# Kernel tuning notes

Hardware: AMD Instinct MI355X
Metric: run time of the kernel (lower is better)

Reference implementation:

```python
import jax, jax.numpy as jnp
import numpy as np

L = 2000          # number of residues (sequence length)
FEATURES_L = 2048 # config.features_L pad target
W = 7             # config.window_size
D = 54            # per-residue feature dim after bert_lin
H = 3             # attention heads
HD = D // H       # head dim = 18
CH = 32           # conv hidden channels
KS = (3, 5, 7)    # config.kernels


def setup_inputs() -> dict:
    key = jax.random.key(0)
    ks = jax.random.split(key, 20)
    n = lambda k, s, sc=0.02: jax.random.normal(k, s, jnp.float32) * sc
    return {
        'beft_f': jax.random.normal(ks[0], (L, 1024), jnp.float32),
        'pssm_f': jax.random.normal(ks[1], (L, 20), jnp.float32),
        'hmm_f': jax.random.normal(ks[2], (L, 30), jnp.float32),
        'dssp_f': jax.random.normal(ks[3], (L, 14), jnp.float32),
        'W_bert': n(ks[4], (1024, D)), 'b_bert': jnp.zeros((D,), jnp.float32),
        'ln_g1': jnp.ones((D,), jnp.float32), 'ln_b1': jnp.zeros((D,), jnp.float32),
        'ln_g2': jnp.ones((D,), jnp.float32), 'ln_b2': jnp.zeros((D,), jnp.float32),
        'conv1_w': n(ks[5], (CH, 1, 3, 1), 0.1), 'conv1_b': n(ks[6], (CH,), 0.1),
        'prelu_a': jnp.array(0.25, jnp.float32),
        'conv2_w': n(ks[7], (CH, 1, 5, 1), 0.1), 'conv2_b': n(ks[8], (CH,), 0.1),
        'conv3_w': n(ks[9], (CH, 1, 7, 1), 0.1), 'conv3_b': n(ks[10], (CH,), 0.1),
        'W1': n(ks[11], (972, 256)), 'b1': jnp.zeros((256,), jnp.float32),
        'W2': n(ks[12], (CH * 256, 256)), 'b2': jnp.zeros((256,), jnp.float32),
    }


def _ln(x, g, b, eps=1e-5):
    m = x.mean(-1, keepdims=True)
    v = ((x - m) ** 2).mean(-1, keepdims=True)
    return (x - m) * jax.lax.rsqrt(v + eps) * g + b


def _attn(x, g, b):
    # x: (L, W, D); no qkv projections, no 1/sqrt(d) scaling (as in source)
    qh = x.reshape(x.shape[0], W, H, HD)
    s = jnp.einsum('bqhd,bkhd->bhqk', qh, qh)
    p = jax.nn.softmax(s, axis=-1)
    o = jnp.einsum('bhqk,bkhd->bqhd', p, qh).reshape(x.shape[0], W, D)
    return _ln(o, g, b)


def _conv_branch(x, w, bias, k, act):
    pad = (k - 1) // 2
    c = jax.lax.conv_general_dilated(x, w, (1, 1), ((pad, pad), (0, 0)),
                                     dimension_numbers=('NCHW', 'OIHW', 'NCHW'))
    c = act(c + bias[None, :, None, None])
    c = jax.lax.reduce_window(c, -jnp.inf, jax.lax.max,
                              (1, 1, k, 1), (1, 1, 1, 1), 'VALID')
    return c.reshape(c.shape[0], CH, -1)  # (FEATURES_L, 32, (W-k+1)*2D)


def _forward(beft_f, W_bert, b_bert, ln_g1, ln_b1, ln_g2, ln_b2,
             conv1_w, conv1_b, prelu_a, conv2_w, conv2_b, conv3_w, conv3_b,
             W1, b1, W2, b2):
    f = beft_f @ W_bert + b_bert  # (L, 54)
    # sliding-window gather replicating the source python loop exactly:
    # interior rows i in (W, L-W): window = f[i-4 : i+3]; boundary rows: [f[i], 0...0]
    i = jnp.arange(L)
    j = jnp.arange(W)
    gidx = jnp.clip(i[:, None] - (W // 2 + 1) + j[None, :], 0, L - 1)
    win_int = f[gidx]                                   # (L, 7, 54)
    win_bnd = jnp.zeros((L, W, D), f.dtype).at[:, 0].set(f)
    boundary = (i <= W) | (i + W >= L)
    new_f = jnp.where(boundary[:, None, None], win_bnd, win_int)
    sf = _attn(new_f, ln_g1, ln_b1)
    sf = _attn(sf, ln_g2, ln_b2)
    cat = jnp.concatenate([new_f, sf], axis=2)          # (L, 7, 108)
    x = jnp.pad(cat, ((0, FEATURES_L - L), (0, 0), (0, 0)))[:, None]  # (FL,1,7,108)
    prelu = lambda z: jnp.where(z >= 0, z, prelu_a * z)
    feats = jnp.concatenate([
        _conv_branch(x, conv1_w, conv1_b, KS[0], prelu),
        _conv_branch(x, conv2_w, conv2_b, KS[1], jax.nn.relu),
        _conv_branch(x, conv3_w, conv3_b, KS[2], jax.nn.relu)], axis=2)  # (FL,32,972)
    y = feats[:L] @ W1 + b1                             # (L, 32, 256)
    y = y.reshape(L, CH * 256) @ W2 + b2                # (L, 256)
    return jnp.where(y >= 0, y, 0.01 * y)               # leaky_relu


def reference(beft_f, pssm_f, hmm_f, dssp_f, W_bert, b_bert, ln_g1, ln_b1,
              ln_g2, ln_b2, conv1_w, conv1_b, prelu_a, conv2_w, conv2_b,
              conv3_w, conv3_b, W1, b1, W2, b2):
    # pssm_f / hmm_f / dssp_f are accepted but unused in the source forward
    return _forward(beft_f, W_bert, b_bert, ln_g1, ln_b1, ln_g2, ln_b2,
                    conv1_w, conv1_b, prelu_a, conv2_w, conv2_b,
                    conv3_w, conv3_b, W1, b1, W2, b2)
```

## Files before the change

### kernel.cpp

```cpp
#include <hip/hip_runtime.h>

#define L_RES 2000
#define DF 54
#define WIN 7

typedef short bf16x8 __attribute__((ext_vector_type(8)));
typedef float f32x4 __attribute__((ext_vector_type(4)));
typedef unsigned short ushort8v __attribute__((ext_vector_type(8)));

__device__ __forceinline__ unsigned short f2bf(float f) {
    unsigned int u = __float_as_uint(f);
    unsigned int r = (u + 0x7FFFu + ((u >> 16) & 1u)) >> 16;
    return (unsigned short)r;
}
__device__ __forceinline__ float bf2f(unsigned short h) {
    return __uint_as_float(((unsigned int)h) << 16);
}
__device__ __forceinline__ void gload16(const unsigned short* g, unsigned short* l) {
    __builtin_amdgcn_global_load_lds(
        (const __attribute__((address_space(1))) void*)g,
        (__attribute__((address_space(3))) void*)l, 16, 0, 0);
}

__global__ __launch_bounds__(256) void b2t_build(const float* __restrict__ Wb,
                                                 unsigned short* __restrict__ B2T) {
    int idx = blockIdx.x * 256 + threadIdx.x;
    int n = idx / 3072, col = idx % 3072;
    int seg = col >> 10, k = col & 1023;
    unsigned short r = 0;
    if (n < DF) {
        float v = Wb[(size_t)k * DF + n];
        unsigned short hi = f2bf(v);
        r = (seg < 2) ? hi : f2bf(v - bf2f(hi));
    }
    B2T[idx] = r;
}

__global__ __launch_bounds__(256) void bert_mfma(const float* __restrict__ beft,
                                                 const unsigned short* __restrict__ B2T,
                                                 float* __restrict__ bpart) {
    __shared__ unsigned short ldsA[128 * 64];
    __shared__ unsigned short ldsB[64 * 64];
    int t = threadIdx.x, w = t >> 6, lane = t & 63;
    int m0 = blockIdx.x * 128;
    int z = blockIdx.y;
    int koff = z * 768;
    int wr = w >> 1, wc = w & 1;
    int arow = lane & 15, kgrp = lane >> 4;

    int cj[4], aD[4];
    const float* aF[4];
    bool vald[4];
    #pragma unroll
    for (int j = 0; j < 4; ++j) {
        int s = j * 256 + t, r = s >> 3, c = s & 7;
        cj[j] = c;
        aD[j] = r * 64 + ((c ^ (r & 7)) * 8);
        vald[j] = (m0 + r) < L_RES;
        aF[j] = beft + (size_t)(vald[j] ? (m0 + r) : 0) * 1024;
    }
    const unsigned short* bS[2]; int bD[2];
    #pragma unroll
    for (int j = 0; j < 2; ++j) {
        int s = j * 256 + t, r = s >> 3, c = s & 7;
        bS[j] = B2T + koff + (size_t)r * 3072 + c * 8;
        bD[j] = r * 64 + ((c ^ (r & 7)) * 8);
    }
    f32x4 acc[4][2];
    #pragma unroll
    for (int mi = 0; mi < 4; ++mi)
        #pragma unroll
        for (int ni = 0; ni < 2; ++ni) acc[mi][ni] = (f32x4)(0.f);

    f32x4 va0[4], va1[4];
    ushort8v vb[2];
    #pragma unroll
    for (int j = 0; j < 4; ++j) {
        int x = koff + cj[j] * 8;
        int bc = x & 1023;
        va0[j] = *(const f32x4*)(aF[j] + bc);
        va1[j] = *(const f32x4*)(aF[j] + bc + 4);
    }
    #pragma unroll
    for (int j = 0; j < 2; ++j) vb[j] = *(const ushort8v*)(bS[j]);

    for (int ks = 0; ks < 12; ++ks) {
        __syncthreads();
        #pragma unroll
        for (int j = 0; j < 4; ++j) {
            int x = koff + ks * 64 + cj[j] * 8;
            int seg = x >> 10;
            ushort8v v;
            #pragma unroll
            for (int e = 0; e < 8; ++e) {
                float val = (e < 4) ? va0[j][e] : va1[j][e - 4];
                if (!vald[j]) val = 0.f;
                unsigned short hi = f2bf(val);
                v[e] = (seg == 1) ? f2bf(val - bf2f(hi)) : hi;
            }
            *(ushort8v*)&ldsA[aD[j]] = v;
        }
        #pragma unroll
        for (int j = 0; j < 2; ++j) *(ushort8v*)&ldsB[bD[j]] = vb[j];
        __syncthreads();
        if (ks + 1 < 12) {
            #pragma unroll
            for (int j = 0; j < 4; ++j) {
                int x = koff + (ks + 1) * 64 + cj[j] * 8;
                int bc = x & 1023;
                va0[j] = *(const f32x4*)(aF[j] + bc);
                va1[j] = *(const f32x4*)(aF[j] + bc + 4);
            }
            #pragma unroll
            for (int j = 0; j < 2; ++j) vb[j] = *(const ushort8v*)(bS[j] + (ks + 1) * 64);
        }
        #pragma unroll
        for (int kk = 0; kk < 2; ++kk) {
            int chunk = kk * 4 + kgrp;
            bf16x8 af[4], bfr[2];
            #pragma unroll
            for (int mi = 0; mi < 4; ++mi) {
                int rl = wr * 64 + mi * 16 + arow;
                af[mi] = *(const bf16x8*)&ldsA[rl * 64 + ((chunk ^ (rl & 7)) * 8)];
            }
            #pragma unroll
            for (int ni = 0; ni < 2; ++ni) {
                int rl = wc * 32 + ni * 16 + arow;
                bfr[ni] = *(const bf16x8*)&ldsB[rl * 64 + ((chunk ^ (rl & 7)) * 8)];
            }
            #pragma unroll
            for (int mi = 0; mi < 4; ++mi)
                #pragma unroll
                for (int ni = 0; ni < 2; ++ni)
                    acc[mi][ni] = __builtin_amdgcn_mfma_f32_16x16x32_bf16(af[mi], bfr[ni], acc[mi][ni], 0, 0, 0);
        }
    }
    #pragma unroll
    for (int ni = 0; ni < 2; ++ni) {
        int n = wc * 32 + ni * 16 + arow;
        #pragma unroll
        for (int mi = 0; mi < 4; ++mi)
            #pragma unroll
            for (int r = 0; r < 4; ++r) {
                int m = m0 + wr * 64 + mi * 16 + kgrp * 4 + r;
                bpart[((size_t)z * 2048 + m) * 64 + n] = acc[mi][ni][r];
            }
    }
}

__global__ __launch_bounds__(64) void bert_reduce(const float* __restrict__ bpart,
                                                  const float* __restrict__ bb,
                                                  float* __restrict__ f) {
    int l = blockIdx.x, n = threadIdx.x;
    if (n < DF) {
        float s = bb[n];
        #pragma unroll
        for (int z = 0; z < 4; ++z) s += bpart[((size_t)z * 2048 + l) * 64 + n];
        f[(size_t)l * DF + n] = s;
    }
}

__device__ __forceinline__ void attn_layer(const float (*in)[DF], float (*out)[DF],
                                           float (*s)[WIN][WIN],
                                           const float* __restrict__ g,
                                           const float* __restrict__ b,
                                           float* mm, float* vv, int t) {
    for (int idx = t; idx < 3 * WIN * WIN; idx += 64) {
        int h = idx / 49, r = idx % 49, q = r / WIN, k = r % WIN;
        float sum = 0.f;
        #pragma unroll
        for (int d = 0; d < 18; ++d) sum = fmaf(in[q][h * 18 + d], in[k][h * 18 + d], sum);
        s[h][q][k] = sum;
    }
    __syncthreads();
    for (int idx = t; idx < 3 * WIN; idx += 64) {
        int h = idx / WIN, q = idx % WIN;
        float mx = s[h][q][0];
        #pragma unroll
        for (int k = 1; k < WIN; ++k) mx = fmaxf(mx, s[h][q][k]);
        float e[WIN], sum = 0.f;
        #pragma unroll
        for (int k = 0; k < WIN; ++k) { e[k] = expf(s[h][q][k] - mx); sum += e[k]; }
        float inv = 1.f / sum;
        #pragma unroll
        for (int k = 0; k < WIN; ++k) s[h][q][k] = e[k] * inv;
    }
    __syncthreads();
    for (int idx = t; idx < WIN * DF; idx += 64) {
        int q = idx / DF, c = idx % DF, h = c / 18;
        float sum = 0.f;
        #pragma unroll
        for (int k = 0; k < WIN; ++k) sum = fmaf(s[h][q][k], in[k][c], sum);
        out[q][c] = sum;
    }
    __syncthreads();
    for (int q = t; q < WIN; q += 64) {
        float m = 0.f;
        for (int c = 0; c < DF; ++c) m += out[q][c];
        m *= (1.f / DF);
        float v = 0.f;
        for (int c = 0; c < DF; ++c) { float d0 = out[q][c] - m; v = fmaf(d0, d0, v); }
        v *= (1.f / DF);
        mm[q] = m; vv[q] = rsqrtf(v + 1e-5f);
    }
    __syncthreads();
    for (int idx = t; idx < WIN * DF; idx += 64) {
        int q = idx / DF, c = idx % DF;
        out[q][c] = (out[q][c] - mm[q]) * vv[q] * g[c] + b[c];
    }
    __syncthreads();
}

__global__ __launch_bounds__(64) void window_attn(const float* __restrict__ f,
                                                  const float* __restrict__ g1,
                                                  const float* __restrict__ b1,
                                                  const float* __restrict__ g2,
                                                  const float* __restrict__ b2,
                                                  float* __restrict__ cat) {
    int l = blockIdx.x;
    int t = threadIdx.x;
    __shared__ float w[WIN][DF], o1[WIN][DF], o2[WIN][DF];
    __shared__ float s[3][WIN][WIN];
    __shared__ float mm[WIN], vv[WIN];
    bool boundary = (l <= WIN) || (l + WIN >= L_RES);
    for (int idx = t; idx < WIN * DF; idx += 64) {
        int j = idx / DF, d = idx % DF;
        w[j][d] = boundary ? (j == 0 ? f[(size_t)l * DF + d] : 0.f)
                           : f[(size_t)(l - 4 + j) * DF + d];
    }
    __syncthreads();
    attn_layer(w, o1, s, g1, b1, mm, vv, t);
    attn_layer(o1, o2, s, g2, b2, mm, vv, t);
    for (int idx = t; idx < WIN * DF; idx += 64) {
        int j = idx / DF, d = idx % DF;
        cat[(size_t)l * 756 + j * 108 + d] = w[j][d];
        cat[(size_t)l * 756 + j * 108 + DF + d] = o2[j][d];
    }
}

__global__ __launch_bounds__(256) void transpose_to_bf16(const float* __restrict__ src,
                                                         unsigned short* __restrict__ dst,
                                                         int M, int N, int Mpad) {
    __shared__ float tile[32][33];
    int m0 = blockIdx.x * 32, n0 = blockIdx.y * 32;
    int c = threadIdx.x % 32, r0 = threadIdx.x / 32;
    #pragma unroll
    for (int rr = 0; rr < 4; ++rr) {
        int r = r0 + rr * 8, m = m0 + r;
        tile[r][c] = (m < M) ? src[(size_t)m * N + n0 + c] : 0.f;
    }
    __syncthreads();
    #pragma unroll
    for (int rr = 0; rr < 4; ++rr) {
        int r = r0 + rr * 8;
        dst[(size_t)(n0 + r) * Mpad + m0 + c] = f2bf(tile[c][r]);
    }
}

__global__ __launch_bounds__(256) void w1tp_build(const float* __restrict__ W1,
                                                  unsigned short* __restrict__ P) {
    int idx = blockIdx.x * 256 + threadIdx.x;
    int e = idx & 7, l = (idx >> 3) & 63, g = (idx >> 9) & 31, nb = idx >> 14;
    int ks = g >> 1, kk = g & 1;
    int n = nb * 16 + (l & 15);
    int k = ks * 64 + kk * 32 + (l >> 4) * 8 + e;
    P[idx] = (k < 972) ? f2bf(W1[(size_t)k * 256 + n]) : (unsigned short)0;
}

__global__ __launch_bounds__(256) void conv_pool(
        const float* __restrict__ cat,
        const float* __restrict__ c1w, const float* __restrict__ c1b,
        const float* __restrict__ pa_p,
        const float* __restrict__ c2w, const float* __restrict__ c2b,
        const float* __restrict__ c3w, const float* __restrict__ c3b,
        unsigned short* __restrict__ Ap, int lbase) {
    int bid = blockIdx.x;
    int b = bid >> 2;
    int ch0 = (bid & 3) * 8;
    int l0 = lbase + b * 4;
    int t = threadIdx.x;
    __shared__ float catl[4 * 756];
    for (int i = t; i < 3024; i += 256) catl[i] = cat[(size_t)l0 * 756 + i];
    __syncthreads();
    float pa = pa_p[0];
    unsigned short* base = Ap + (size_t)b * 128 * 1024;
    int res = t >> 6, dp = t & 63;
    if (dp < 54) {
        int d0 = dp * 2;
        const float* cr = catl + res * 756;
        float colA[WIN], colB[WIN];
        #pragma unroll
        for (int h = 0; h < WIN; ++h) {
            colA[h] = cr[h * 108 + d0];
            colB[h] = cr[h * 108 + d0 + 1];
        }
        for (int c = ch0; c < ch0 + 8; ++c) {
            unsigned short* Arow = base + (size_t)(res * 32 + c) * 1024;
            {
                float w0 = c1w[c * 3], w1 = c1w[c * 3 + 1], w2 = c1w[c * 3 + 2];
                float bb = c1b[c];
                float vA[WIN], vB[WIN];
                #pragma unroll
                for (int h = 0; h < WIN; ++h) {
                    float sA = bb, sB = bb;
                    if (h >= 1) { sA = fmaf(w0, colA[h - 1], sA); sB = fmaf(w0, colB[h - 1], sB); }
                    sA = fmaf(w1, colA[h], sA); sB = fmaf(w1, colB[h], sB);
                    if (h <= 5) { sA = fmaf(w2, colA[h + 1], sA); sB = fmaf(w2, colB[h + 1], sB); }
                    vA[h] = sA >= 0.f ? sA : pa * sA;
                    vB[h] = sB >= 0.f ? sB : pa * sB;
                }
                #pragma unroll
                for (int p = 0; p < 5; ++p) {
                    unsigned int ua = f2bf(fmaxf(fmaxf(vA[p], vA[p + 1]), vA[p + 2]));
                    unsigned int ub = f2bf(fmaxf(fmaxf(vB[p], vB[p + 1]), vB[p + 2]));
                    *(unsigned int*)&Arow[p * 108 + d0] = ua | (ub << 16);
                }
            }
            {
                float wg[5], bb = c2b[c];
                #pragma unroll
                for (int x = 0; x < 5; ++x) wg[x] = c2w[c * 5 + x];
                float vA[WIN], vB[WIN];
                #pragma unroll
                for (int h = 0; h < WIN; ++h) {
                    float sA = bb, sB = bb;
                    #pragma unroll
                    for (int x = 0; x < 5; ++x) {
                        int hh = h + x - 2;
                        if (hh >= 0 && hh <= 6) {
                            sA = fmaf(wg[x], colA[hh], sA);
                            sB = fmaf(wg[x], colB[hh], sB);
                        }
                    }
                    vA[h] = fmaxf(sA, 0.f);
                    vB[h] = fmaxf(sB, 0.f);
                }
                #pragma unroll
                for (int p = 0; p < 3; ++p) {
                    float ma = vA[p], mb = vB[p];
                    #pragma unroll
                    for (int r = 1; r < 5; ++r) { ma = fmaxf(ma, vA[p + r]); mb = fmaxf(mb, vB[p + r]); }
                    unsigned int ua = f2bf(ma), ub = f2bf(mb);
                    *(unsigned int*)&Arow[540 + p * 108 + d0] = ua | (ub << 16);
                }
            }
            {
                float wg[7], bb = c3b[c];
                #pragma unroll
                for (int x = 0; x < 7; ++x) wg[x] = c3w[c * 7 + x];
                float ma = 0.f, mb = 0.f;
                #pragma unroll
                for (int h = 0; h < WIN; ++h) {
                    float sA = bb, sB = bb;
                    #pragma unroll
                    for (int x = 0; x < 7; ++x) {
                        int hh = h + x - 3;
                        if (hh >= 0 && hh <= 6) {
                            sA = fmaf(wg[x], colA[hh], sA);
                            sB = fmaf(wg[x], colB[hh], sB);
                        }
                    }
                    ma = fmaxf(ma, sA);
                    mb = fmaxf(mb, sB);
                }
                unsigned int ua = f2bf(fmaxf(ma, 0.f)), ub = f2bf(fmaxf(mb, 0.f));
                *(unsigned int*)&Arow[864 + d0] = ua | (ub << 16);
            }
        }
    }
    for (int i = t; i < 832; i += 256) {
        int r = i / 26, q = i - r * 26;
        int res2 = r >> 3, c2 = ch0 + (r & 7);
        *(unsigned int*)&base[(size_t)(res2 * 32 + c2) * 1024 + 972 + q * 2] = 0u;
    }
}

__global__ __launch_bounds__(256, 2) void gemm1k(
        const unsigned short* __restrict__ A,
        const unsigned short* __restrict__ P,
        const float* __restrict__ b1v,
        unsigned short* __restrict__ y1, long outRowBase) {
    __shared__ unsigned short ldsA[2][128 * 64];
    int t = threadIdx.x, w = t >> 6, lane = t & 63;
    long m0 = (long)blockIdx.x * 128;
    int arow = lane & 15, kgrp = lane >> 4;
    int ra = lane >> 3, cc = lane & 7;
    int csw = (cc ^ ra) * 8;

    const unsigned short* gA[4]; int rb[4];
    #pragma unroll
    for (int j = 0; j < 4; ++j) {
        int rbase = j * 32 + w * 8;
        gA[j] = A + (size_t)(m0 + rbase + ra) * 1024 + csw;
        rb[j] = rbase * 64;
    }
    f32x4 acc[8][4];
    #pragma unroll
    for (int mi = 0; mi < 8; ++mi)
        #pragma unroll
        for (int ni = 0; ni < 4; ++ni) acc[mi][ni] = (f32x4)(0.f);

    #pragma unroll
    for (int j = 0; j < 4; ++j) gload16(gA[j], &ldsA[0][rb[j]]);
    __syncthreads();

    for (int ks = 0; ks < 16; ++ks) {
        int cur = ks & 1;
        bf16x8 bfr[2][4];
        #pragma unroll
        for (int kk = 0; kk < 2; ++kk)
            #pragma unroll
            for (int ni = 0; ni < 4; ++ni)
                bfr[kk][ni] = *(const bf16x8*)&P[(((size_t)(w * 4 + ni) * 32 + ks * 2 + kk) * 64 + lane) * 8];
        if (ks + 1 < 16) {
            #pragma unroll
            for (int j = 0; j < 4; ++j) gload16(gA[j] + (ks + 1) * 64, &ldsA[cur ^ 1][rb[j]]);
        }
        #pragma unroll
        for (int kk = 0; kk < 2; ++kk) {
            int chunk = kk * 4 + kgrp;
            bf16x8 af[8];
            #pragma unroll
            for (int mi = 0; mi < 8; ++mi) {
                int rl = mi * 16 + arow;
                af[mi] = *(const bf16x8*)&ldsA[cur][rl * 64 + ((chunk ^ (rl & 7)) * 8)];
            }
            #pragma unroll
            for (int mi = 0; mi < 8; ++mi)
                #pragma unroll
                for (int ni = 0; ni < 4; ++ni)
                    acc[mi][ni] = __builtin_amdgcn_mfma_f32_16x16x32_bf16(af[mi], bfr[kk][ni], acc[mi][ni], 0, 0, 0);
        }
        __syncthreads();
    }
    #pragma unroll
    for (int ni = 0; ni < 4; ++ni) {
        int n = w * 64 + ni * 16 + arow;
        float bv = b1v[n];
        #pragma unroll
        for (int mi = 0; mi < 8; ++mi)
            #pragma unroll
            for (int r = 0; r < 4; ++r) {
                long row = m0 + mi * 16 + kgrp * 4 + r;
                y1[(outRowBase + row) * 256 + n] = f2bf(acc[mi][ni][r] + bv);
            }
    }
}

template<bool EPI_BF16, int ZBITS>
__global__ __launch_bounds__(512) void gemm_tile8(
        const unsigned short* __restrict__ A, long lda,
        const unsigned short* __restrict__ B, long ldb,
        int nk, const float* __restrict__ bias,
        unsigned short* __restrict__ outB, float* __restrict__ outF,
        long outRowBase) {
    __shared__ unsigned short ldsA[128 * 64];
    __shared__ unsigned short ldsB[256 * 64];
    int t = threadIdx.x, w = t >> 6, lane = t & 63;
    int bid = blockIdx.x;
    int z = bid & ((1 << ZBITS) - 1);
    long m0 = (long)(bid >> ZBITS) * 128;
    long koff = (long)z * (long)nk * 64;
    A += koff; B += koff;
    int wr = w >> 2, wc = w & 3;
    int arow = lane & 15, kgrp = lane >> 4;
    int ra = lane >> 3, cc = lane & 7;
    int csw = (cc ^ ra) * 8;

    const unsigned short* gA[2]; const unsigned short* gB[4];
    unsigned short* dA[2]; unsigned short* dB[4];
    #pragma unroll
    for (int j = 0; j < 2; ++j) {
        int rbase = j * 64 + w * 8;
        gA[j] = A + (size_t)(m0 + rbase + ra) * lda + csw;
        dA[j] = &ldsA[rbase * 64];
    }
    #pragma unroll
    for (int j = 0; j < 4; ++j) {
        int rbase = j * 64 + w * 8;
        gB[j] = B + (size_t)(rbase + ra) * ldb + csw;
        dB[j] = &ldsB[rbase * 64];
    }
    f32x4 acc[4][4];
    #pragma unroll
    for (int mi = 0; mi < 4; ++mi)
        #pragma unroll
        for (int ni = 0; ni < 4; ++ni) acc[mi][ni] = (f32x4)(0.f);

    for (int ks = 0; ks < nk; ++ks) {
        #pragma unroll
        for (int j = 0; j < 2; ++j) gload16(gA[j] + ks * 64, dA[j]);
        #pragma unroll
        for (int j = 0; j < 4; ++j) gload16(gB[j] + ks * 64, dB[j]);
        __syncthreads();
        #pragma unroll
        for (int kk = 0; kk < 2; ++kk) {
            int chunk = kk * 4 + kgrp;
            bf16x8 af[4], bfr[4];
            #pragma unroll
            for (int mi = 0; mi < 4; ++mi) {
                int rl = wr * 64 + mi * 16 + arow;
                af[mi] = *(const bf16x8*)&ldsA[rl * 64 + ((chunk ^ (rl & 7)) * 8)];
            }
            #pragma unroll
            for (int ni = 0; ni < 4; ++ni) {
                int rl = wc * 64 + ni * 16 + arow;
                bfr[ni] = *(const bf16x8*)&ldsB[rl * 64 + ((chunk ^ (rl & 7)) * 8)];
            }
            #pragma unroll
            for (int mi = 0; mi < 4; ++mi)
                #pragma unroll
                for (int ni = 0; ni < 4; ++ni)
                    acc[mi][ni] = __builtin_amdgcn_mfma_f32_16x16x32_bf16(af[mi], bfr[ni], acc[mi][ni], 0, 0, 0);
        }
        __syncthreads();
    }
    #pragma unroll
    for (int ni = 0; ni < 4; ++ni) {
        int n = wc * 64 + ni * 16 + arow;
        float bv = EPI_BF16 ? bias[n] : 0.f;
        #pragma unroll
        for (int mi = 0; mi < 4; ++mi)
            #pragma unroll
            for (int r = 0; r < 4; ++r) {
                long m = m0 + wr * 64 + mi * 16 + kgrp * 4 + r;
                if (EPI_BF16)
                    outB[(outRowBase + m) * 256 + n] = f2bf(acc[mi][ni][r] + bv);
                else
                    outF[((long)z * 2048 + m) * 256 + n] = acc[mi][ni][r];
            }
    }
}

__global__ __launch_bounds__(256) void reduce2(const float* __restrict__ part,
                                               const float* __restrict__ b2v,
                                               float* __restrict__ out) {
    int l = blockIdx.x, n = threadIdx.x;
    float sum = b2v[n];
    #pragma unroll
    for (int s = 0; s < 16; ++s) sum += part[((size_t)s * 2048 + l) * 256 + n];
    out[(size_t)l * 256 + n] = sum >= 0.f ? sum : 0.01f * sum;
}

extern "C" void kernel_launch(void* const* d_in, const int* in_sizes, int n_in,
                              void* d_out, int out_size, void* d_ws, size_t ws_size,
                              hipStream_t stream) {
    const float* beft = (const float*)d_in[0];
    const float* Wb  = (const float*)d_in[4];
    const float* bb  = (const float*)d_in[5];
    const float* g1  = (const float*)d_in[6];
    const float* b1  = (const float*)d_in[7];
    const float* g2  = (const float*)d_in[8];
    const float* b2  = (const float*)d_in[9];
    const float* c1w = (const float*)d_in[10];
    const float* c1b = (const float*)d_in[11];
    const float* pa  = (const float*)d_in[12];
    const float* c2w = (const float*)d_in[13];
    const float* c2b = (const float*)d_in[14];
    const float* c3w = (const float*)d_in[15];
    const float* c3b = (const float*)d_in[16];
    const float* W1  = (const float*)d_in[17];
    const float* b1v = (const float*)d_in[18];
    const float* W2  = (const float*)d_in[19];
    const float* b2v = (const float*)d_in[20];
    float* out = (float*)d_out;
    char* ws = (char*)d_ws;

    float*          f    = (float*)(ws + 0);
    float*          cat  = (float*)(ws + 524288);
    unsigned short* W1Tp = (unsigned short*)(ws + 8388608);
    unsigned short* W2T  = (unsigned short*)(ws + 8912896);
    unsigned short* y1   = (unsigned short*)(ws + 13107200);
    unsigned short* B2T  = (unsigned short*)(ws + 25690112);
    float*          bpart= (float*)(ws + 46661632);
    unsigned short* Ap   = (unsigned short*)(ws + 46661632);
    float*          part = (float*)(ws + 46661632);

    long avail = (long)ws_size - 46661632L;
    long tpc = avail / (128L * 1024L * 2L);
    if (tpc < 1) tpc = 1;
    if (tpc > 500) tpc = 500;

    b2t_build<<<768, 256, 0, stream>>>(Wb, B2T);
    bert_mfma<<<dim3(16, 4), 256, 0, stream>>>(beft, B2T, bpart);
    bert_reduce<<<L_RES, 64, 0, stream>>>(bpart, bb, f);
    window_attn<<<L_RES, 64, 0, stream>>>(f, g1, b1, g2, b2, cat);
    w1tp_build<<<1024, 256, 0, stream>>>(W1, W1Tp);
    transpose_to_bf16<<<dim3(256, 8), 256, 0, stream>>>(W2, W2T, 8192, 256, 8192);

    for (long t0 = 0; t0 < 500; t0 += tpc) {
        long nt = (500 - t0 < tpc) ? (500 - t0) : tpc;
        conv_pool<<<(int)(nt * 4), 256, 0, stream>>>(cat, c1w, c1b, pa, c2w, c2b,
                                                     c3w, c3b, Ap, (int)(t0 * 4));
        gemm1k<<<(int)nt, 256, 0, stream>>>(Ap, W1Tp, b1v, y1, t0 * 128);
    }
    gemm_tile8<false, 4><<<256, 512, 0, stream>>>(
        y1, 8192, W2T, 8192, 8, nullptr, nullptr, part, 0);
    reduce2<<<L_RES, 256, 0, stream>>>(part, b2v, out);
}
```

Measured before the change: 148.3 us.

## Merge weight-prep kernels, fold bert reduce into attention, prefetch B in gemm1k

Merges the two weight-conversion kernels into a single launch and drops the bert_reduce kernel by having window_attn sum the split-K partials and bias itself. The gemm1k main loop is restructured into a two-stage register double buffer for the B fragments, loading the next step's B alongside the LDS staging of A. This removes two launches and an intermediate buffer round trip, and aims to hide B global-load latency behind MFMA work. The cost is redundant partial-sum reads in window_attn (each residue is read by up to seven windows) and higher register pressure in gemm1k.

```diff
diff --git a/kernel.cpp b/kernel.cpp
--- a/kernel.cpp
+++ b/kernel.cpp
@@ -22,18 +22,30 @@
         (__attribute__((address_space(3))) void*)l, 16, 0, 0);
 }
 
-__global__ __launch_bounds__(256) void b2t_build(const float* __restrict__ Wb,
-                                                 unsigned short* __restrict__ B2T) {
-    int idx = blockIdx.x * 256 + threadIdx.x;
-    int n = idx / 3072, col = idx % 3072;
-    int seg = col >> 10, k = col & 1023;
-    unsigned short r = 0;
-    if (n < DF) {
-        float v = Wb[(size_t)k * DF + n];
-        unsigned short hi = f2bf(v);
-        r = (seg < 2) ? hi : f2bf(v - bf2f(hi));
-    }
-    B2T[idx] = r;
+__global__ __launch_bounds__(256) void prep_w(const float* __restrict__ Wb,
+                                              unsigned short* __restrict__ B2T,
+                                              const float* __restrict__ W1,
+                                              unsigned short* __restrict__ P) {
+    int bid = blockIdx.x;
+    if (bid < 768) {
+        int idx = bid * 256 + threadIdx.x;
+        int n = idx / 3072, col = idx % 3072;
+        int seg = col >> 10, k = col & 1023;
+        unsigned short r = 0;
+        if (n < DF) {
+            float v = Wb[(size_t)k * DF + n];
+            unsigned short hi = f2bf(v);
+            r = (seg < 2) ? hi : f2bf(v - bf2f(hi));
+        }
+        B2T[idx] = r;
+    } else {
+        int idx = (bid - 768) * 256 + threadIdx.x;
+        int e = idx & 7, l = (idx >> 3) & 63, g = (idx >> 9) & 31, nb = idx >> 14;
+        int ks = g >> 1, kk = g & 1;
+        int n = nb * 16 + (l & 15);
+        int k = ks * 64 + kk * 32 + (l >> 4) * 8 + e;
+        P[idx] = (k < 972) ? f2bf(W1[(size_t)k * 256 + n]) : (unsigned short)0;
+    }
 }
 
 __global__ __launch_bounds__(256) void bert_mfma(const float* __restrict__ beft,
@@ -148,18 +160,6 @@
     }
 }
 
-__global__ __launch_bounds__(64) void bert_reduce(const float* __restrict__ bpart,
-                                                  const float* __restrict__ bb,
-                                                  float* __restrict__ f) {
-    int l = blockIdx.x, n = threadIdx.x;
-    if (n < DF) {
-        float s = bb[n];
-        #pragma unroll
-        for (int z = 0; z < 4; ++z) s += bpart[((size_t)z * 2048 + l) * 64 + n];
-        f[(size_t)l * DF + n] = s;
-    }
-}
-
 __device__ __forceinline__ void attn_layer(const float (*in)[DF], float (*out)[DF],
                                            float (*s)[WIN][WIN],
                                            const float* __restrict__ g,
@@ -211,7 +211,8 @@
     __syncthreads();
 }
 
-__global__ __launch_bounds__(64) void window_attn(const float* __restrict__ f,
+__global__ __launch_bounds__(64) void window_attn(const float* __restrict__ bpart,
+                                                  const float* __restrict__ bb,
                                                   const float* __restrict__ g1,
                                                   const float* __restrict__ b1,
                                                   const float* __restrict__ g2,
@@ -225,8 +226,14 @@
     bool boundary = (l <= WIN) || (l + WIN >= L_RES);
     for (int idx = t; idx < WIN * DF; idx += 64) {
         int j = idx / DF, d = idx % DF;
-        w[j][d] = boundary ? (j == 0 ? f[(size_t)l * DF + d] : 0.f)
-                           : f[(size_t)(l - 4 + j) * DF + d];
+        float v = 0.f;
+        if (!boundary || j == 0) {
+            int lsrc = boundary ? l : (l - 4 + j);
+            v = bb[d];
+            #pragma unroll
+            for (int z = 0; z < 4; ++z) v += bpart[((size_t)z * 2048 + lsrc) * 64 + d];
+        }
+        w[j][d] = v;
     }
     __syncthreads();
     attn_layer(w, o1, s, g1, b1, mm, vv, t);
@@ -255,16 +262,6 @@
         int r = r0 + rr * 8;
         dst[(size_t)(n0 + r) * Mpad + m0 + c] = f2bf(tile[c][r]);
     }
-}
-
-__global__ __launch_bounds__(256) void w1tp_build(const float* __restrict__ W1,
-                                                  unsigned short* __restrict__ P) {
-    int idx = blockIdx.x * 256 + threadIdx.x;
-    int e = idx & 7, l = (idx >> 3) & 63, g = (idx >> 9) & 31, nb = idx >> 14;
-    int ks = g >> 1, kk = g & 1;
-    int n = nb * 16 + (l & 15);
-    int k = ks * 64 + kk * 32 + (l >> 4) * 8 + e;
-    P[idx] = (k < 972) ? f2bf(W1[(size_t)k * 256 + n]) : (unsigned short)0;
 }
 
 __global__ __launch_bounds__(256) void conv_pool(
@@ -400,22 +397,18 @@
         #pragma unroll
         for (int ni = 0; ni < 4; ++ni) acc[mi][ni] = (f32x4)(0.f);
 
-    #pragma unroll
-    for (int j = 0; j < 4; ++j) gload16(gA[j], &ldsA[0][rb[j]]);
-    __syncthreads();
-
-    for (int ks = 0; ks < 16; ++ks) {
-        int cur = ks & 1;
-        bf16x8 bfr[2][4];
+    auto loadB = [&](bf16x8 (&dst)[2][4], int ksv) {
         #pragma unroll
         for (int kk = 0; kk < 2; ++kk)
             #pragma unroll
             for (int ni = 0; ni < 4; ++ni)
-                bfr[kk][ni] = *(const bf16x8*)&P[(((size_t)(w * 4 + ni) * 32 + ks * 2 + kk) * 64 + lane) * 8];
-        if (ks + 1 < 16) {
-            #pragma unroll
-            for (int j = 0; j < 4; ++j) gload16(gA[j] + (ks + 1) * 64, &ldsA[cur ^ 1][rb[j]]);
-        }
+                dst[kk][ni] = *(const bf16x8*)&P[(((size_t)(w * 4 + ni) * 32 + ksv * 2 + kk) * 64 + lane) * 8];
+    };
+    auto stage = [&](int ksv, int buf) {
+        #pragma unroll
+        for (int j = 0; j < 4; ++j) gload16(gA[j] + ksv * 64, &ldsA[buf][rb[j]]);
+    };
+    auto compute = [&](int buf, bf16x8 (&b)[2][4]) {
         #pragma unroll
         for (int kk = 0; kk < 2; ++kk) {
             int chunk = kk * 4 + kgrp;
@@ -423,14 +416,33 @@
             #pragma unroll
             for (int mi = 0; mi < 8; ++mi) {
                 int rl = mi * 16 + arow;
-                af[mi] = *(const bf16x8*)&ldsA[cur][rl * 64 + ((chunk ^ (rl & 7)) * 8)];
+                af[mi] = *(const bf16x8*)&ldsA[buf][rl * 64 + ((chunk ^ (rl & 7)) * 8)];
             }
             #pragma unroll
             for (int mi = 0; mi < 8; ++mi)
                 #pragma unroll
                 for (int ni = 0; ni < 4; ++ni)
-                    acc[mi][ni] = __builtin_amdgcn_mfma_f32_16x16x32_bf16(af[mi], bfr[kk][ni], acc[mi][ni], 0, 0, 0);
-        }
+                    acc[mi][ni] = __builtin_amdgcn_mfma_f32_16x16x32_bf16(af[mi], b[kk][ni], acc[mi][ni], 0, 0, 0);
+        }
+    };
+
+    bf16x8 bA[2][4], bB[2][4];
+    loadB(bA, 0);
+    stage(0, 0);
+    __syncthreads();
+
+    #pragma unroll 1
+    for (int ks2 = 0; ks2 < 8; ++ks2) {
+        int ks = ks2 * 2;
+        loadB(bB, ks + 1);
+        stage(ks + 1, 1);
+        compute(0, bA);
+        __syncthreads();
+        if (ks + 2 < 16) {
+            loadB(bA, ks + 2);
+            stage(ks + 2, 0);
+        }
+        compute(1, bB);
         __syncthreads();
     }
     #pragma unroll
@@ -566,7 +578,6 @@
     float* out = (float*)d_out;
     char* ws = (char*)d_ws;
 
-    float*          f    = (float*)(ws + 0);
     float*          cat  = (float*)(ws + 524288);
     unsigned short* W1Tp = (unsigned short*)(ws + 8388608);
     unsigned short* W2T  = (unsigned short*)(ws + 8912896);
@@ -581,11 +592,9 @@
     if (tpc < 1) tpc = 1;
     if (tpc > 500) tpc = 500;
 
-    b2t_build<<<768, 256, 0, stream>>>(Wb, B2T);
+    prep_w<<<1792, 256, 0, stream>>>(Wb, B2T, W1, W1Tp);
     bert_mfma<<<dim3(16, 4), 256, 0, stream>>>(beft, B2T, bpart);
-    bert_reduce<<<L_RES, 64, 0, stream>>>(bpart, bb, f);
-    window_attn<<<L_RES, 64, 0, stream>>>(f, g1, b1, g2, b2, cat);
-    w1tp_build<<<1024, 256, 0, stream>>>(W1, W1Tp);
+    window_attn<<<L_RES, 64, 0, stream>>>(bpart, bb, g1, b1, g2, b2, cat);
     transpose_to_bf16<<<dim3(256, 8), 256, 0, stream>>>(W2, W2T, 8192, 256, 8192);
 
     for (long t0 = 0; t0 < 500; t0 += tpc) {
```

Measured after the change: 149.2 us. About the same (+0.7%).
